# Kernel tuning notes

Hardware: AMD Instinct MI355X
Metric: run time of the kernel (lower is better)

Reference implementation:

```python
import jax, jax.numpy as jnp
import numpy as np

# Geometry from the hard-coded `options` tensor
VIEWS, DETS = 160, 640
H, W = 416, 416
D_IMG = 0.006641            # image pixel size
D_DET = 0.012858            # detector bin size
ANG0 = 0.0
D_ANG = 0.009817477 * 4     # = 2*pi/160 (full scan)
S2R = 5.95                  # source-to-rotation-center distance
D2R = 4.906                 # detector-to-rotation-center distance
VIRDET = D_DET * S2R / (S2R + D2R)   # detector rescaled to isocenter (virtual detector)
PI = float(np.pi)
COEF = PI / VIEWS
BATCH = 32


def setup_inputs() -> dict:
    key = jax.random.key(0)
    projection = jax.random.normal(key, (BATCH, 1, VIEWS, DETS), dtype=jnp.float32)

    # Ramp filter (Ram-Lak, spatial domain), length 2*dets-1, exactly as in torch __init__
    x = np.arange(2 * DETS - 1) - DETS + 1
    x_safe = np.where(x == 0, 1, x).astype(np.float64)
    filt = np.where(np.abs(x) % 2 == 1,
                    -1.0 / (PI * PI * x_safe * x_safe * VIRDET * VIRDET),
                    0.0)
    filt[x == 0] = 1.0 / (4.0 * VIRDET * VIRDET)
    filt = jnp.asarray(filt.reshape(1, 1, 1, -1), dtype=jnp.float32)

    # Cosine (fan-beam) pre-weighting, detector bin centers at (i - dets/2 + 0.5)*virdet
    u = (np.arange(DETS) - DETS / 2 + 0.5) * VIRDET
    wv = S2R / np.sqrt(S2R ** 2 + u ** 2) * VIRDET
    w = jnp.asarray(wv.reshape(1, 1, 1, -1), dtype=jnp.float32)

    return {"projection": projection, "w": w, "filt": filt}


def _backproject(p):
    """Pixel-driven equidistant fan-beam backprojection.
    p: filtered sinogram [B, 1, VIEWS, DETS] -> recon [B, 1, H, W].
    """
    betas = ANG0 + D_ANG * jnp.arange(VIEWS, dtype=jnp.float32)
    xs = (jnp.arange(W, dtype=jnp.float32) - (W - 1) / 2.0) * D_IMG   # [W]
    ys = ((H - 1) / 2.0 - jnp.arange(H, dtype=jnp.float32)) * D_IMG   # [H]
    Xg, Yg = jnp.meshgrid(xs, ys)   # both [H, W]

    pv = jnp.moveaxis(p, 2, 0)  # [VIEWS, B, 1, DETS]

    def step(acc, inp):
        beta, pb = inp                      # pb: [B, 1, DETS]
        cb, sb = jnp.cos(beta), jnp.sin(beta)
        d = Xg * cb + Yg * sb               # pixel component toward source
        r = -Xg * sb + Yg * cb              # perpendicular component
        U = S2R - d                         # source-to-pixel depth
        # detector coordinate at isocenter -> fractional bin index
        idx = (S2R * r / U) / VIRDET + (DETS - 1) / 2.0   # [H, W]
        valid = (idx >= 0.0) & (idx <= DETS - 1)
        i0 = jnp.clip(jnp.floor(idx), 0, DETS - 2).astype(jnp.int32)
        frac = jnp.clip(idx - i0.astype(jnp.float32), 0.0, 1.0)
        # irregular gather + linear interpolation: [B,1,H,W]
        v = pb[:, :, i0] * (1.0 - frac) + pb[:, :, i0 + 1] * frac
        wgt = jnp.where(valid, (S2R / U) ** 2, 0.0)       # distance weighting
        return acc + wgt * v, None

    init = jnp.zeros((p.shape[0], 1, H, W), dtype=p.dtype)
    acc, _ = jax.lax.scan(step, init, (betas, pv))
    return acc


def reference(projection, w, filt):
    # 1) cosine weighting (elementwise broadcast over detector axis)
    p = projection * w
    p = jax.lax.conv_general_dilated(
        p, filt, window_strides=(1, 1),
        padding=((0, 0), (DETS - 1, DETS - 1)),
        dimension_numbers=("NCHW", "OIHW", "NCHW"))
    # 3) geometric backprojection + angular step normalization
    return COEF * _backproject(p)
```

## Files before the change

kernel.cpp:

```cpp
#include <hip/hip_runtime.h>

#define VIEWS 160
#define DETS  640
#define H_IMG 416
#define W_IMG 416
#define BATCH 32

constexpr double D_IMG_D  = 0.006641;
constexpr double D_DET_D  = 0.012858;
constexpr double S2R_D    = 5.95;
constexpr double D2R_D    = 4.906;
constexpr double VIRDET_D = D_DET_D * S2R_D / (S2R_D + D2R_D);
constexpr double PI_D     = 3.14159265358979323846;

typedef __fp16 __attribute__((ext_vector_type(2))) h2f;

#define TILES_X 13
#define TILES_Y 52
#define NTILES  (TILES_X * TILES_Y)
#define NB      64
#define ZSPLIT  2


__device__ __forceinline__ float dot2_acc(h2f p, h2f w, float acc) {
#if __has_builtin(__builtin_amdgcn_fdot2)
    return __builtin_amdgcn_fdot2(p, w, acc, false);
#else
    return fmaf((float)p.x, (float)w.x, fmaf((float)p.y, (float)w.y, acc));
#endif
}

__global__ __launch_bounds__(256) void init_kernel(float* __restrict__ vcs,
                                                   int* __restrict__ bs_tab,
                                                   float4* __restrict__ out4) {
    int t    = threadIdx.x;
    int tile = blockIdx.x;
    if (t < VIEWS) {
        int v = t;
        float dang = (float)(0.009817477 * 4.0);
        float beta = dang * (float)v;
        float cb = cosf(beta), sb = sinf(beta);
        float K  = (float)(S2R_D / VIRDET_D);
        if (tile == 0) {
            ((float4*)vcs)[v] = make_float4(cb, sb, -K * sb, K * cb);
        }
        int ty = tile / TILES_X, tx = tile - ty * TILES_X;
        float XL = ((float)(tx * 32) - 207.5f) * (float)D_IMG_D;
        float XR = ((float)(tx * 32 + 31) - 207.5f) * (float)D_IMG_D;
        float YT = (207.5f - (float)(ty * 8)) * (float)D_IMG_D;
        float YB = (207.5f - (float)(ty * 8 + 7)) * (float)D_IMG_D;
        float m = 1e30f;
#define CORNER(Xc, Yc) { \
        float r_ = -(Xc) * sb + (Yc) * cb; \
        float U_ = (float)S2R_D - (Xc) * cb - (Yc) * sb; \
        float ix = fmaf(K, r_ / U_, 319.5f); \
        m = fminf(m, ix); }
        CORNER(XL, YT); CORNER(XR, YT); CORNER(XL, YB); CORNER(XR, YB);
#undef CORNER
        int bs = (int)floorf(m) - 2;
        bs = max(0, min(DETS - NB, bs)) & ~1;
        bs_tab[tile * VIEWS + v] = bs;
    }
    size_t base = (size_t)tile * 2048 + t;
    float4 z = make_float4(0.f, 0.f, 0.f, 0.f);
    #pragma unroll
    for (int i = 0; i < 8; ++i) out4[base + (size_t)i * 256] = z;
}

#define FT 320
#define RPAD 24
#define RSTR 209
__global__ __launch_bounds__(FT) void filter_kernel(
    const float* __restrict__ proj, const float* __restrict__ w,
    const float* __restrict__ filt, unsigned int* __restrict__ pf2) {
    __shared__ float4 s_in[4 * RSTR];
    __shared__ float  s_f[2 * DETS];
    __shared__ unsigned int s_out[2 * DETS];

    int t = threadIdx.x;
    int g = blockIdx.x;
    int group4 = g / 160;
    int v = g - group4 * 160;

    for (int e = t; e < 4 * RSTR; e += FT) {
        int ri = e / RSTR, c4 = e - ri * RSTR;
        float4 pv = make_float4(0.f, 0.f, 0.f, 0.f);
        if (c4 >= RPAD && c4 < RPAD + 160) {
            int b = group4 * 4 + ri;
            pv = ((const float4*)(proj + ((size_t)b * VIEWS + v) * DETS))[c4 - RPAD];
            float4 wv = ((const float4*)w)[c4 - RPAD];
            pv.x *= wv.x; pv.y *= wv.y; pv.z *= wv.z; pv.w *= wv.w;
        }
        s_in[e] = pv;
    }
    for (int e = t; e < 2 * DETS; e += FT) s_f[e] = (e < 2 * DETS - 1) ? filt[e] : 0.f;
    __syncthreads();

    int sub = (t >= 160) ? 1 : 0;
    int tj  = t - sub * 160;

    const float4* f4  = (const float4*)s_f;
    const float4* in4 = &s_in[sub * 2 * RSTR + tj];
    float4 o0 = {0,0,0,0}, o1 = {0,0,0,0};
    float4 fp = f4[135];
    #pragma unroll 2
    for (int u = 0; u < 50; ++u) {
        float4 fn = f4[136 + u];
        {
            float4 iv = in4[0 * RSTR + u];
            o0.x = fmaf(iv.x, fp.w, o0.x); o0.x = fmaf(iv.y, fn.x, o0.x);
            o0.x = fmaf(iv.z, fn.y, o0.x); o0.x = fmaf(iv.w, fn.z, o0.x);
            o0.y = fmaf(iv.x, fp.z, o0.y); o0.y = fmaf(iv.y, fp.w, o0.y);
            o0.y = fmaf(iv.z, fn.x, o0.y); o0.y = fmaf(iv.w, fn.y, o0.y);
            o0.z = fmaf(iv.x, fp.y, o0.z); o0.z = fmaf(iv.y, fp.z, o0.z);
            o0.z = fmaf(iv.z, fp.w, o0.z); o0.z = fmaf(iv.w, fn.x, o0.z);
            o0.w = fmaf(iv.x, fp.x, o0.w); o0.w = fmaf(iv.y, fp.y, o0.w);
            o0.w = fmaf(iv.z, fp.z, o0.w); o0.w = fmaf(iv.w, fp.w, o0.w);
        }
        {
            float4 iv = in4[1 * RSTR + u];
            o1.x = fmaf(iv.x, fp.w, o1.x); o1.x = fmaf(iv.y, fn.x, o1.x);
            o1.x = fmaf(iv.z, fn.y, o1.x); o1.x = fmaf(iv.w, fn.z, o1.x);
            o1.y = fmaf(iv.x, fp.z, o1.y); o1.y = fmaf(iv.y, fp.w, o1.y);
            o1.y = fmaf(iv.z, fn.x, o1.y); o1.y = fmaf(iv.w, fn.y, o1.y);
            o1.z = fmaf(iv.x, fp.y, o1.z); o1.z = fmaf(iv.y, fp.z, o1.z);
            o1.z = fmaf(iv.z, fp.w, o1.z); o1.z = fmaf(iv.w, fn.x, o1.z);
            o1.w = fmaf(iv.x, fp.x, o1.w); o1.w = fmaf(iv.y, fp.y, o1.w);
            o1.w = fmaf(iv.z, fp.z, o1.w); o1.w = fmaf(iv.w, fp.w, o1.w);
        }
        fp = fn;
    }

    float coef = (float)((PI_D / (double)VIEWS) * S2R_D * S2R_D);
    auto h0 = __builtin_amdgcn_cvt_pkrtz(o0.x * coef, o1.x * coef);
    auto h1 = __builtin_amdgcn_cvt_pkrtz(o0.y * coef, o1.y * coef);
    auto h2 = __builtin_amdgcn_cvt_pkrtz(o0.z * coef, o1.z * coef);
    auto h3 = __builtin_amdgcn_cvt_pkrtz(o0.w * coef, o1.w * coef);
    uint4 pk = make_uint4(__builtin_bit_cast(unsigned int, h0),
                          __builtin_bit_cast(unsigned int, h1),
                          __builtin_bit_cast(unsigned int, h2),
                          __builtin_bit_cast(unsigned int, h3));
    *(uint4*)&s_out[sub * DETS + 4 * tj] = pk;
    __syncthreads();

    unsigned int* dstv = pf2 + (size_t)v * 20480 + (size_t)group4 * 4;
    #pragma unroll
    for (int cc = 0; cc < 2; ++cc) {
        int k  = 2 * t + cc;
        int k1 = k + 1;
        unsigned int u0  = s_out[k];
        unsigned int u0n = (k1 < DETS) ? s_out[k1] : 0u;
        unsigned int u1  = s_out[DETS + k];
        unsigned int u1n = (k1 < DETS) ? s_out[DETS + k1] : 0u;
        uint4 o;
        o.x = __builtin_amdgcn_perm(u0n, u0, 0x05040100u);
        o.y = __builtin_amdgcn_perm(u0n, u0, 0x07060302u);
        o.z = __builtin_amdgcn_perm(u1n, u1, 0x05040100u);
        o.w = __builtin_amdgcn_perm(u1n, u1, 0x07060302u);
        *(uint4*)(dstv + (size_t)cc * 10240 + (size_t)t * 32) = o;
    }
}

__device__ __forceinline__ void gld_lds16(const char* g, char* l) {
    __builtin_amdgcn_global_load_lds(
        (const __attribute__((address_space(1))) unsigned int*)g,
        (__attribute__((address_space(3))) unsigned int*)l, 16, 0, 0);
}

__global__ __launch_bounds__(256, 6) void bp_kernel(
    const unsigned int* __restrict__ pf2, const float* __restrict__ vcs,
    const int* __restrict__ bs_tab, float* __restrict__ out) {
    __shared__ alignas(16) unsigned int s_buf[2 * 2048];

    int t    = threadIdx.x;
    int half = blockIdx.z;
    int tile = blockIdx.y * TILES_X + blockIdx.x;
    int x    = blockIdx.x * 32 + (t & 31);
    int y    = blockIdx.y * 8 + (t >> 5);

    float X  = ((float)x - 207.5f) * (float)D_IMG_D;
    float Yv = (207.5f - (float)y) * (float)D_IMG_D;

    int vstart = half * (VIEWS / ZSPLIT);
    const float4* vc4 = (const float4*)vcs + vstart;
    const int*    bsp = bs_tab + tile * VIEWS + vstart;
    const char*   pfb = (const char*)pf2 + (size_t)vstart * 81920;

    int r_s  = (t >> 3) & 31;
    int k_s  = t & 7;
    int toff0 = r_s * 128 + ((k_s ^ (r_s & 7)) << 4);
    int wvbase = (t >> 6) << 10;

    float acc[32];
    #pragma unroll
    for (int b = 0; b < 32; ++b) acc[b] = 0.f;

    #define STAGE(c) do { \
        int bsd = bsp[(c)]; \
        const char* src = pfb + (size_t)(c) * 81920 + (size_t)bsd * 64; \
        char* dst = (char*)s_buf + (((c) & 1) << 13) + wvbase; \
        gld_lds16(src + toff0, dst); \
        gld_lds16(src + 40960 + toff0, dst + 4096); \
    } while (0)

    STAGE(0);
    __syncthreads();

    int nv = VIEWS / ZSPLIT;
    for (int c = 0; c < nv; ++c) {
        if (c + 1 < nv) STAGE(c + 1);

        float4 a   = vc4[c];
        int    bsc = bsp[c];
        float U    = fmaf(-X, a.x, fmaf(-Yv, a.y, (float)S2R_D));
        float num  = fmaf(X, a.z, Yv * a.w);
        float ru   = __builtin_amdgcn_rcpf(U);
        float idx  = fmaf(num, ru, 319.5f);
        float idxc = __builtin_amdgcn_fmed3f(idx, 0.f, 639.f);
        float i0f  = fminf(idxc, 638.0f);
        int   i0   = (int)i0f;
        float frac = idxc - truncf(i0f);
        float w2   = ru * ru;
        float wgt  = (idx == idxc) ? w2 : 0.f;
        float w1f  = wgt * frac;
        float w0f  = wgt - w1f;
        h2f w01    = __builtin_amdgcn_cvt_pkrtz(w0f, w1f);

        int rel = min(max(i0 - bsc, 0), NB - 2);
        int cc  = rel & 1;
        int rr  = rel >> 1;
        int b2  = ((c & 1) << 13) + (cc << 12) + (rr << 7) + ((rr & 7) << 4);
        const char* pbase = (const char*)s_buf;
        #pragma unroll
        for (int k = 0; k < 8; ++k) {
            uint4 q = *(const uint4*)(pbase + (b2 ^ (k << 4)));
            acc[4 * k + 0] = dot2_acc(__builtin_bit_cast(h2f, q.x), w01, acc[4 * k + 0]);
            acc[4 * k + 1] = dot2_acc(__builtin_bit_cast(h2f, q.y), w01, acc[4 * k + 1]);
            acc[4 * k + 2] = dot2_acc(__builtin_bit_cast(h2f, q.z), w01, acc[4 * k + 2]);
            acc[4 * k + 3] = dot2_acc(__builtin_bit_cast(h2f, q.w), w01, acc[4 * k + 3]);
        }
        __syncthreads();
    }
    #undef STAGE

    float* ob = out + (size_t)y * W_IMG + x;
    #pragma unroll
    for (int b = 0; b < 32; ++b)
        unsafeAtomicAdd(ob + (size_t)b * (H_IMG * W_IMG), acc[b]);
}

extern "C" void kernel_launch(void* const* d_in, const int* in_sizes, int n_in,
                              void* d_out, int out_size, void* d_ws, size_t ws_size,
                              hipStream_t stream) {
    const float* proj = (const float*)d_in[0];
    const float* w    = (const float*)d_in[1];
    const float* filt = (const float*)d_in[2];
    float* out = (float*)d_out;

    float*        vcs    = (float*)d_ws;
    int*          bs_tab = (int*)((char*)d_ws + 4096);
    unsigned int* pf2    = (unsigned int*)((char*)d_ws + 442368);

    init_kernel<<<NTILES, 256, 0, stream>>>(vcs, bs_tab, (float4*)out);
    filter_kernel<<<(BATCH / 4) * VIEWS, FT, 0, stream>>>(proj, w, filt, pf2);
    bp_kernel<<<dim3(TILES_X, TILES_Y, ZSPLIT), 256, 0, stream>>>(pf2, vcs, bs_tab, out);
}
```

Before: 203.0 us.

## Split views three ways, interleave filtered layout by detector, raise occupancy hint

The backprojection grid now splits the view range into three uneven chunks instead of two, giving more blocks and more atomic accumulation into the output. The filtered sinogram layout changes from an even/odd detector split to a contiguous per-detector layout, which simplifies the LDS address computation in the inner loop and the staging source offsets. The launch bound minimum blocks per CU rises from 6 to 8, which may constrain registers for the 32 accumulators. Extra atomics and possible register pressure are the trade-offs.

```diff
diff --git a/kernel.cpp b/kernel.cpp
--- a/kernel.cpp
+++ b/kernel.cpp
@@ -19,7 +19,7 @@
 #define TILES_Y 52
 #define NTILES  (TILES_X * TILES_Y)
 #define NB      64
-#define ZSPLIT  2
+#define ZSPLIT  3
 
 
 __device__ __forceinline__ float dot2_acc(h2f p, h2f w, float acc) {
@@ -72,7 +72,7 @@
 #define RSTR 209
 __global__ __launch_bounds__(FT) void filter_kernel(
     const float* __restrict__ proj, const float* __restrict__ w,
-    const float* __restrict__ filt, unsigned int* __restrict__ pf2) {
+    const float* __restrict__ filt, unsigned int* __restrict__ pf3) {
     __shared__ float4 s_in[4 * RSTR];
     __shared__ float  s_f[2 * DETS];
     __shared__ unsigned int s_out[2 * DETS];
@@ -143,21 +143,21 @@
     *(uint4*)&s_out[sub * DETS + 4 * tj] = pk;
     __syncthreads();
 
-    unsigned int* dstv = pf2 + (size_t)v * 20480 + (size_t)group4 * 4;
+    unsigned int* dstv = pf3 + (size_t)v * 20480 + (size_t)group4 * 4;
     #pragma unroll
     for (int cc = 0; cc < 2; ++cc) {
-        int k  = 2 * t + cc;
-        int k1 = k + 1;
-        unsigned int u0  = s_out[k];
-        unsigned int u0n = (k1 < DETS) ? s_out[k1] : 0u;
-        unsigned int u1  = s_out[DETS + k];
-        unsigned int u1n = (k1 < DETS) ? s_out[DETS + k1] : 0u;
+        int j  = 2 * t + cc;
+        int j1 = j + 1;
+        unsigned int u0  = s_out[j];
+        unsigned int u0n = (j1 < DETS) ? s_out[j1] : 0u;
+        unsigned int u1  = s_out[DETS + j];
+        unsigned int u1n = (j1 < DETS) ? s_out[DETS + j1] : 0u;
         uint4 o;
         o.x = __builtin_amdgcn_perm(u0n, u0, 0x05040100u);
         o.y = __builtin_amdgcn_perm(u0n, u0, 0x07060302u);
         o.z = __builtin_amdgcn_perm(u1n, u1, 0x05040100u);
         o.w = __builtin_amdgcn_perm(u1n, u1, 0x07060302u);
-        *(uint4*)(dstv + (size_t)cc * 10240 + (size_t)t * 32) = o;
+        *(uint4*)(dstv + (size_t)j * 32) = o;
     }
 }
 
@@ -167,13 +167,13 @@
         (__attribute__((address_space(3))) unsigned int*)l, 16, 0, 0);
 }
 
-__global__ __launch_bounds__(256, 6) void bp_kernel(
-    const unsigned int* __restrict__ pf2, const float* __restrict__ vcs,
+__global__ __launch_bounds__(256, 8) void bp_kernel(
+    const unsigned int* __restrict__ pf3, const float* __restrict__ vcs,
     const int* __restrict__ bs_tab, float* __restrict__ out) {
     __shared__ alignas(16) unsigned int s_buf[2 * 2048];
 
     int t    = threadIdx.x;
-    int half = blockIdx.z;
+    int zc   = blockIdx.z;
     int tile = blockIdx.y * TILES_X + blockIdx.x;
     int x    = blockIdx.x * 32 + (t & 31);
     int y    = blockIdx.y * 8 + (t >> 5);
@@ -181,10 +181,12 @@
     float X  = ((float)x - 207.5f) * (float)D_IMG_D;
     float Yv = (207.5f - (float)y) * (float)D_IMG_D;
 
-    int vstart = half * (VIEWS / ZSPLIT);
+    int vstart = (zc * VIEWS) / ZSPLIT;
+    int vend   = ((zc + 1) * VIEWS) / ZSPLIT;
+    int nv     = vend - vstart;
     const float4* vc4 = (const float4*)vcs + vstart;
     const int*    bsp = bs_tab + tile * VIEWS + vstart;
-    const char*   pfb = (const char*)pf2 + (size_t)vstart * 81920;
+    const char*   pfb = (const char*)pf3 + (size_t)vstart * 81920;
 
     int r_s  = (t >> 3) & 31;
     int k_s  = t & 7;
@@ -197,16 +199,15 @@
 
     #define STAGE(c) do { \
         int bsd = bsp[(c)]; \
-        const char* src = pfb + (size_t)(c) * 81920 + (size_t)bsd * 64; \
+        const char* src = pfb + (size_t)(c) * 81920 + (size_t)bsd * 128 + toff0; \
         char* dst = (char*)s_buf + (((c) & 1) << 13) + wvbase; \
-        gld_lds16(src + toff0, dst); \
-        gld_lds16(src + 40960 + toff0, dst + 4096); \
+        gld_lds16(src, dst); \
+        gld_lds16(src + 4096, dst + 4096); \
     } while (0)
 
     STAGE(0);
     __syncthreads();
 
-    int nv = VIEWS / ZSPLIT;
     for (int c = 0; c < nv; ++c) {
         if (c + 1 < nv) STAGE(c + 1);
 
@@ -227,9 +228,7 @@
         h2f w01    = __builtin_amdgcn_cvt_pkrtz(w0f, w1f);
 
         int rel = min(max(i0 - bsc, 0), NB - 2);
-        int cc  = rel & 1;
-        int rr  = rel >> 1;
-        int b2  = ((c & 1) << 13) + (cc << 12) + (rr << 7) + ((rr & 7) << 4);
+        int b2  = ((c & 1) << 13) + (rel << 7) + ((rel & 7) << 4);
         const char* pbase = (const char*)s_buf;
         #pragma unroll
         for (int k = 0; k < 8; ++k) {
@@ -259,9 +258,9 @@
 
     float*        vcs    = (float*)d_ws;
     int*          bs_tab = (int*)((char*)d_ws + 4096);
-    unsigned int* pf2    = (unsigned int*)((char*)d_ws + 442368);
+    unsigned int* pf3    = (unsigned int*)((char*)d_ws + 442368);
 
     init_kernel<<<NTILES, 256, 0, stream>>>(vcs, bs_tab, (float4*)out);
-    filter_kernel<<<(BATCH / 4) * VIEWS, FT, 0, stream>>>(proj, w, filt, pf2);
-    bp_kernel<<<dim3(TILES_X, TILES_Y, ZSPLIT), 256, 0, stream>>>(pf2, vcs, bs_tab, out);
-}
+    filter_kernel<<<(BATCH / 4) * VIEWS, FT, 0, stream>>>(proj, w, filt, pf3);
+    bp_kernel<<<dim3(TILES_X, TILES_Y, ZSPLIT), 256, 0, stream>>>(pf3, vcs, bs_tab, out);
+}
```

Measured after the change: 191.9 us. 5.5% less time.
